# Performance work log

Hardware: AMD Instinct MI355X
Metric: run time of the kernel (lower is better)

## Reference

```python
import jax, jax.numpy as jnp
import numpy as np

BSZ, SEQ, DK = 16, 2048, 64


def setup_inputs() -> dict:
    key = jax.random.key(0)
    kq, kk, kv, kp = jax.random.split(key, 4)
    Q = jax.random.normal(kq, (BSZ, SEQ, DK), dtype=jnp.float32)
    K = jax.random.normal(kk, (BSZ, SEQ, DK), dtype=jnp.float32)
    V = jax.random.normal(kv, (BSZ, SEQ, DK), dtype=jnp.float32)
    # learned relative-position key projection, Parameter(dk, sizeSeq)
    Krelpos = jax.random.normal(kp, (DK, SEQ), dtype=jnp.float32) * (1.0 / np.sqrt(DK))
    return {"Q": Q, "K": K, "V": V, "Krelpos": Krelpos}


def reference(Q, K, V, Krelpos):
    b, S, dk = Q.shape
    # content scores: [b, S, S]
    QK = jnp.einsum('bsd,btd->bst', Q, K)
    # relative-position bias via skew trick
    QP = jnp.einsum('bsd,dt->bst', Q, Krelpos)                     # [b, S, S]
    QP = jnp.concatenate([jnp.zeros((b, S, 1), QP.dtype), QP], axis=2)  # [b, S, S+1]
    QK = QK + QP.reshape(b, S + 1, S)[:, 1:, :]                    # skewed -> [b, S, S]
    # causal mask: -inf strictly above diagonal
    causal = jnp.tril(jnp.ones((S, S), dtype=bool))
    mask = jnp.where(causal, jnp.zeros((), QK.dtype), -jnp.inf)
    A = jax.nn.softmax(QK / jnp.sqrt(jnp.asarray(dk, QK.dtype)) + mask, axis=2)
    # dropout p=0.0 -> identity
    return jnp.einsum('bst,btd->bsd', A, V)
```

## Files before the change

### kernel.cpp

```cpp
#include <hip/hip_runtime.h>
#include <math.h>

#define BSZ 16
#define SEQ 2048
#define DKD 64
#define NTH 256

typedef __attribute__((ext_vector_type(8))) short bf16x8;
typedef __attribute__((ext_vector_type(8))) short short8;
typedef __attribute__((ext_vector_type(4))) float f32x4;

__device__ __forceinline__ short f2bf(float x) {
  union { float f; unsigned u; } c; c.f = x;
  unsigned r = c.u + 0x7fffu + ((c.u >> 16) & 1u);
  return (short)(r >> 16);
}

__device__ __forceinline__ int pkbf(float hi, float lo) {
  return (int)__builtin_amdgcn_perm(__float_as_uint(hi), __float_as_uint(lo), 0x07060302u);
}

#define GLD16(gsrc, ldst)                                                                  \
  __builtin_amdgcn_global_load_lds((const __attribute__((address_space(1))) void*)(gsrc), \
                                   (__attribute__((address_space(3))) void*)(ldst), 16, 0, 0)

#define CH(row, c8) (((row) << 3) + ((c8) ^ ((row) & 7)))


__launch_bounds__(NTH)
__global__ void pre_convert(const float* __restrict__ K, const float* __restrict__ V,
                            const float* __restrict__ P, short* __restrict__ Kbf,
                            short* __restrict__ VTbf, short* __restrict__ PTbf,
                            float* __restrict__ Ozero, float* __restrict__ Lzero) {
  __shared__ short T[64 * 65];
  const int blk = blockIdx.x;
  const int tid = threadIdx.x;
  if (blk < 1024) {
    const int b = blk >> 6, ch = blk & 63;
    const float* Kb = K + ((size_t)(b * SEQ + ch * 32)) * DKD;
    const float* Vb = V + ((size_t)(b * SEQ + ch * 32)) * DKD;
    const int r = tid >> 3, c8 = (tid & 7) << 3;
    float4 a0 = *(const float4*)(Kb + r * DKD + c8);
    float4 a1 = *(const float4*)(Kb + r * DKD + c8 + 4);
    short8 ko;
    ko[0] = f2bf(a0.x); ko[1] = f2bf(a0.y); ko[2] = f2bf(a0.z); ko[3] = f2bf(a0.w);
    ko[4] = f2bf(a1.x); ko[5] = f2bf(a1.y); ko[6] = f2bf(a1.z); ko[7] = f2bf(a1.w);
    *(short8*)(Kbf + ((size_t)(b * SEQ + ch * 32 + r)) * DKD + c8) = ko;
    float4 v0 = *(const float4*)(Vb + r * DKD + c8);
    float4 v1 = *(const float4*)(Vb + r * DKD + c8 + 4);
    T[(c8 + 0) * 33 + r] = f2bf(v0.x); T[(c8 + 1) * 33 + r] = f2bf(v0.y);
    T[(c8 + 2) * 33 + r] = f2bf(v0.z); T[(c8 + 3) * 33 + r] = f2bf(v0.w);
    T[(c8 + 4) * 33 + r] = f2bf(v1.x); T[(c8 + 5) * 33 + r] = f2bf(v1.y);
    T[(c8 + 6) * 33 + r] = f2bf(v1.z); T[(c8 + 7) * 33 + r] = f2bf(v1.w);
    __syncthreads();
    const int d = tid >> 2, q8 = (tid & 3) << 3;
    short8 w;
    #pragma unroll
    for (int j = 0; j < 8; ++j) w[j] = T[d * 33 + q8 + j];
    *(short8*)(VTbf + ((size_t)(b * DKD + d)) * SEQ + ch * 32 + q8) = w;
  } else if (blk < 1056) {
    const int c0 = (blk - 1024) * 64;
    const int d = tid >> 2, cc4 = (tid & 3) << 4;
    #pragma unroll
    for (int j4 = 0; j4 < 4; ++j4) {
      const int c = cc4 + j4 * 4;
      float4 pv = *(const float4*)(P + (size_t)d * SEQ + c0 + c);
      T[(c + 0) * 65 + d] = f2bf(pv.x);
      T[(c + 1) * 65 + d] = f2bf(pv.y);
      T[(c + 2) * 65 + d] = f2bf(pv.z);
      T[(c + 3) * 65 + d] = f2bf(pv.w);
    }
    __syncthreads();
    const int c = tid >> 2, d4 = (tid & 3) << 4;
    short8 w0, w1;
    #pragma unroll
    for (int j = 0; j < 8; ++j) { w0[j] = T[c * 65 + d4 + j]; w1[j] = T[c * 65 + d4 + 8 + j]; }
    short* Po = PTbf + ((size_t)(c0 + c)) * DKD + d4;
    *(short8*)(Po + 0) = w0;
    *(short8*)(Po + 8) = w1;
  } else if (blk == 1056) {
    short8 z = {0, 0, 0, 0, 0, 0, 0, 0};
    short* Po = PTbf + (size_t)SEQ * DKD + tid * 16;
    *(short8*)(Po + 0) = z;
    *(short8*)(Po + 8) = z;
  } else if (blk < 1569) {
    const int u = blk - 1057;
    float4 z = {0.f, 0.f, 0.f, 0.f};
    float4* p = (float4*)(Ozero + (size_t)u * 4096 + tid * 16);
    p[0] = z; p[1] = z; p[2] = z; p[3] = z;
  } else {
    const int u = blk - 1569;
    float4 z = {0.f, 0.f, 0.f, 0.f};
    float4* p = (float4*)(Lzero + (size_t)u * 4096 + tid * 16);
    p[0] = z; p[1] = z; p[2] = z; p[3] = z;
  }
}

__launch_bounds__(NTH, 4)
__global__ void attn_split(const float* __restrict__ Q,
                           const short* __restrict__ Kbf,
                           const short* __restrict__ VTbf,
                           const short* __restrict__ PTbf,
                           float* __restrict__ Oacc,
                           float* __restrict__ Lacc) {
  __shared__ __align__(16) short smem[16384];
  short* Ks  = smem;
  short* VsT = smem + 4096;
  short* PsT = smem + 8192;

  const int tid = threadIdx.x;
  const int lane = tid & 63;
  const int wave = tid >> 6;
  const int l16 = lane & 15;
  const int quad = lane >> 4;

  const int i = blockIdx.x;
  const int qidx = i >> 5;
  const int s = i & 31;
  const int b = s & 15;
  const int h = s >> 4;
  const int qt = (qidx < 16) ? (31 - qidx) : (qidx - 16);
  const int r0 = qt * 64;
  const int m = (qt + 2) >> 1;
  const int kt0 = h ? m : 0;
  const int kt1 = h ? (qt + 1) : m;
  const float SC = 0.125f * 1.4426950408889634f;

  bf16x8 aq[2];
  {
    const float* Qr = Q + ((size_t)(b * SEQ + r0 + wave * 16 + l16)) * DKD + quad * 8;
    #pragma unroll
    for (int ks = 0; ks < 2; ++ks) {
      float4 x = *(const float4*)(Qr + ks * 32);
      float4 y = *(const float4*)(Qr + ks * 32 + 4);
      bf16x8 t;
      t[0] = f2bf(x.x * SC); t[1] = f2bf(x.y * SC); t[2] = f2bf(x.z * SC); t[3] = f2bf(x.w * SC);
      t[4] = f2bf(y.x * SC); t[5] = f2bf(y.y * SC); t[6] = f2bf(y.z * SC); t[7] = f2bf(y.w * SC);
      aq[ks] = t;
    }
  }

  int gsrc[4];
  bool gcar[4];
  #pragma unroll
  for (int r = 0; r < 4; ++r) {
    int o = 15 - (quad * 4 + r);
    int ss = l16 + o;
    gsrc[r] = (quad << 4) | (ss & 15);
    gcar[r] = (ss >= 16);
  }

  union i4v { int4 i; bf16x8 v; };
  i4v ONESu; ONESu.i = make_int4(0x3F803F80, 0x3F803F80, 0x3F803F80, 0x3F803F80);
  i4v S0u, S1u;
  S0u.i = make_int4(0, 0, 0, 0);
  S1u.i = make_int4(0, 0, 0, 0);
  if (quad == (l16 >> 2)) {
    const int j = l16 & 3;
    const int val = 0x3F80 << ((j & 1) * 16);
    if (j < 2) { S0u.i.x = val; S1u.i.z = val; }
    else       { S0u.i.y = val; S1u.i.w = val; }
  }

  f32x4 oacc[4];
  #pragma unroll
  for (int t = 0; t < 4; ++t)
    #pragma unroll
    for (int j = 0; j < 4; ++j) oacc[t][j] = 0.f;
  f32x4 bl;
  #pragma unroll
  for (int j = 0; j < 4; ++j) bl[j] = 0.f;

  const int Blo0 = 31 - qt;

  for (int kt = kt0; kt < kt1; ++kt) {
    const int j0 = kt * 64;
    __syncthreads();

    #pragma unroll
    for (int half = 0; half < 2; ++half) {
      const int ii = wave * 2 + half;
      const int j = ii * 64 + lane;
      {
        const int k = j >> 3, c8 = (j & 7) ^ (k & 7);
        GLD16(Kbf + ((size_t)(b * SEQ + j0 + k)) * DKD + c8 * 8, Ks + ii * 512);
      }
      {
        const int d = j >> 3, c8 = (j & 7) ^ (d & 7);
        GLD16(VTbf + ((size_t)(b * DKD + d)) * SEQ + j0 + c8 * 8, VsT + ii * 512);
      }
    }
    {
      const int Bg = Blo0 + kt + 1;
      #pragma unroll
      for (int half = 0; half < 2; ++half) {
        const int ii = wave * 2 + half;
        const int j = ii * 64 + lane;
        const int c = j >> 3, c8 = (j & 7) ^ (c & 7);
        GLD16(PTbf + ((size_t)(Bg * 64 + c)) * DKD + c8 * 8,
              PsT + ((Bg & 1) << 12) + ii * 512);
      }
      if (kt == kt0) {
        const int Bl = Blo0 + kt0;
        #pragma unroll
        for (int half = 0; half < 2; ++half) {
          const int ii = wave * 2 + half;
          const int j = ii * 64 + lane;
          const int c = j >> 3, c8 = (j & 7) ^ (c & 7);
          GLD16(PTbf + ((size_t)(Bl * 64 + c)) * DKD + c8 * 8,
                PsT + ((Bl & 1) << 12) + ii * 512);
        }
      }
    }
    __syncthreads();

    f32x4 sacc[4];
    #pragma unroll
    for (int t = 0; t < 4; ++t)
      #pragma unroll
      for (int j = 0; j < 4; ++j) sacc[t][j] = 0.f;
    #pragma unroll
    for (int ks = 0; ks < 2; ++ks)
      #pragma unroll
      for (int t = 0; t < 4; ++t) {
        bf16x8 bk = *(const bf16x8*)&Ks[CH(t * 16 + l16, ks * 4 + quad) << 3];
        sacc[t] = __builtin_amdgcn_mfma_f32_16x16x32_bf16(aq[ks], bk, sacc[t], 0, 0, 0);
      }

    float g[5][4];
    #pragma unroll
    for (int tt = 0; tt < 5; ++tt) {
      f32x4 bacc;
      #pragma unroll
      for (int j = 0; j < 4; ++j) bacc[j] = 0.f;
      const int c = (tt + 3 - wave) * 16 + l16;
      const int pan = (Blo0 + kt + (c >> 6)) & 1;
      const int pr = c & 63;
      #pragma unroll
      for (int ks = 0; ks < 2; ++ks) {
        bf16x8 bp = *(const bf16x8*)&PsT[(pan << 12) + (CH(pr, ks * 4 + quad) << 3)];
        bacc = __builtin_amdgcn_mfma_f32_16x16x32_bf16(aq[ks], bp, bacc, 0, 0, 0);
      }
      #pragma unroll
      for (int r = 0; r < 4; ++r) g[tt][r] = __shfl(bacc[r], gsrc[r], 64);
    }

    const bool diag = (kt == qt);
    float e[4][4];
    #pragma unroll
    for (int t = 0; t < 4; ++t)
      #pragma unroll
      for (int r = 0; r < 4; ++r) {
        float sc = sacc[t][r] + (gcar[r] ? g[t + 1][r] : g[t][r]);
        if (diag && (t * 16 + l16 > wave * 16 + quad * 4 + r)) sc = -INFINITY;
        e[t][r] = exp2f(sc);
      }

    i4v ap0, ap1;
    ap0.i.x = pkbf(e[0][1], e[0][0]); ap0.i.y = pkbf(e[0][3], e[0][2]);
    ap0.i.z = pkbf(e[1][1], e[1][0]); ap0.i.w = pkbf(e[1][3], e[1][2]);
    ap1.i.x = pkbf(e[2][1], e[2][0]); ap1.i.y = pkbf(e[2][3], e[2][2]);
    ap1.i.z = pkbf(e[3][1], e[3][0]); ap1.i.w = pkbf(e[3][3], e[3][2]);

    f32x4 zero4;
    #pragma unroll
    for (int j = 0; j < 4; ++j) zero4[j] = 0.f;
    f32x4 Dt[4];
    Dt[0] = __builtin_amdgcn_mfma_f32_16x16x32_bf16(ap0.v, S0u.v, zero4, 0, 0, 0);
    Dt[1] = __builtin_amdgcn_mfma_f32_16x16x32_bf16(ap0.v, S1u.v, zero4, 0, 0, 0);
    Dt[2] = __builtin_amdgcn_mfma_f32_16x16x32_bf16(ap1.v, S0u.v, zero4, 0, 0, 0);
    Dt[3] = __builtin_amdgcn_mfma_f32_16x16x32_bf16(ap1.v, S1u.v, zero4, 0, 0, 0);

    i4v bp0, bp1;
    bp0.i.x = pkbf(Dt[0][1], Dt[0][0]); bp0.i.y = pkbf(Dt[0][3], Dt[0][2]);
    bp0.i.z = pkbf(Dt[1][1], Dt[1][0]); bp0.i.w = pkbf(Dt[1][3], Dt[1][2]);
    bp1.i.x = pkbf(Dt[2][1], Dt[2][0]); bp1.i.y = pkbf(Dt[2][3], Dt[2][2]);
    bp1.i.z = pkbf(Dt[3][1], Dt[3][0]); bp1.i.w = pkbf(Dt[3][3], Dt[3][2]);

    #pragma unroll
    for (int tp = 0; tp < 2; ++tp) {
      const bf16x8 bpk = tp ? bp1.v : bp0.v;
      bl = __builtin_amdgcn_mfma_f32_16x16x32_bf16(ONESu.v, bpk, bl, 0, 0, 0);
      #pragma unroll
      for (int dt = 0; dt < 4; ++dt) {
        const int row = dt * 16 + l16;
        ushort4 lo = *(const ushort4*)&VsT[(CH(row, tp * 4 + (quad >> 1)) << 3) + (quad & 1) * 4];
        ushort4 hi = *(const ushort4*)&VsT[(CH(row, tp * 4 + 2 + (quad >> 1)) << 3) + (quad & 1) * 4];
        bf16x8 av;
        av[0] = (short)lo.x; av[1] = (short)lo.y; av[2] = (short)lo.z; av[3] = (short)lo.w;
        av[4] = (short)hi.x; av[5] = (short)hi.y; av[6] = (short)hi.z; av[7] = (short)hi.w;
        oacc[dt] = __builtin_amdgcn_mfma_f32_16x16x32_bf16(av, bpk, oacc[dt], 0, 0, 0);
      }
    }
  }

  __syncthreads();
  float* Te = (float*)smem;
  #pragma unroll
  for (int dt = 0; dt < 4; ++dt)
    #pragma unroll
    for (int r = 0; r < 4; ++r)
      Te[(wave * 16 + l16) * 65 + dt * 16 + quad * 4 + r] = oacc[dt][r];
  __syncthreads();
  {
    float* Ob = Oacc + ((size_t)(b * SEQ + r0)) * DKD;
    #pragma unroll
    for (int j = 0; j < 16; ++j) {
      const int idx = j * NTH + tid;
      const int row = idx >> 6, col = idx & 63;
      unsafeAtomicAdd(&Ob[(size_t)row * DKD + col], Te[row * 65 + col]);
    }
    if (quad == 0)
      unsafeAtomicAdd(&Lacc[b * SEQ + r0 + wave * 16 + l16], bl[0]);
  }
}

__launch_bounds__(NTH)
__global__ void norm_out(float* __restrict__ O, const float* __restrict__ L) {
  const int tid = threadIdx.x;
  const int row = blockIdx.x * 16 + (tid >> 4);
  const int c4 = (tid & 15) << 2;
  const float rl = 1.0f / L[row];
  float4* p = (float4*)(O + (size_t)row * DKD + c4);
  float4 v = *p;
  v.x *= rl; v.y *= rl; v.z *= rl; v.w *= rl;
  *p = v;
}

extern "C" void kernel_launch(void* const* d_in, const int* in_sizes, int n_in,
                              void* d_out, int out_size, void* d_ws, size_t ws_size,
                              hipStream_t stream) {
  const float* Q = (const float*)d_in[0];
  const float* K = (const float*)d_in[1];
  const float* V = (const float*)d_in[2];
  const float* P = (const float*)d_in[3];
  float* O = (float*)d_out;

  short* Kbf = (short*)d_ws;
  short* VTbf = (short*)((char*)d_ws + 4194304);
  short* PTbf = (short*)((char*)d_ws + 8388608);
  float* Lacc = (float*)((char*)d_ws + 8658944);

  hipLaunchKernelGGL(pre_convert, dim3(1577), dim3(NTH), 0, stream,
                     K, V, P, Kbf, VTbf, PTbf, O, Lacc);
  hipLaunchKernelGGL(attn_split, dim3(1024), dim3(NTH), 0, stream,
                     Q, Kbf, VTbf, PTbf, O, Lacc);
  hipLaunchKernelGGL(norm_out, dim3(BSZ * SEQ / 16), dim3(NTH), 0, stream, O, Lacc);
}
```

Baseline: 134.6 us.

## Split KV range four ways and fuse normalization via last-block counter

Each query tile's key range now goes to four blocks instead of two, doubling the grid for better load balance and occupancy. A per-tile atomic counter lets the last finishing block divide the accumulated output by the softmax sum, which removes the separate norm_out launch. The VT layout is permuted so the PV operand loads as a single 16-byte LDS read. In exchange there are more atomic adds to O and L and an extra threadfence plus counter atomic per block.

```diff
diff --git a/kernel.cpp b/kernel.cpp
--- a/kernel.cpp
+++ b/kernel.cpp
@@ -31,7 +31,8 @@
 __global__ void pre_convert(const float* __restrict__ K, const float* __restrict__ V,
                             const float* __restrict__ P, short* __restrict__ Kbf,
                             short* __restrict__ VTbf, short* __restrict__ PTbf,
-                            float* __restrict__ Ozero, float* __restrict__ Lzero) {
+                            float* __restrict__ Ozero, float* __restrict__ Lzero,
+                            int* __restrict__ cnt) {
   __shared__ short T[64 * 65];
   const int blk = blockIdx.x;
   const int tid = threadIdx.x;
@@ -53,11 +54,14 @@
     T[(c8 + 4) * 33 + r] = f2bf(v1.x); T[(c8 + 5) * 33 + r] = f2bf(v1.y);
     T[(c8 + 6) * 33 + r] = f2bf(v1.z); T[(c8 + 7) * 33 + r] = f2bf(v1.w);
     __syncthreads();
-    const int d = tid >> 2, q8 = (tid & 3) << 3;
+    const int d = tid >> 2, qg = tid & 3;
     short8 w;
     #pragma unroll
-    for (int j = 0; j < 8; ++j) w[j] = T[d * 33 + q8 + j];
-    *(short8*)(VTbf + ((size_t)(b * DKD + d)) * SEQ + ch * 32 + q8) = w;
+    for (int j = 0; j < 4; ++j) {
+      w[j]     = T[d * 33 + qg * 4 + j];
+      w[4 + j] = T[d * 33 + 16 + qg * 4 + j];
+    }
+    *(short8*)(VTbf + ((size_t)(b * DKD + d)) * SEQ + ch * 32 + qg * 8) = w;
   } else if (blk < 1056) {
     const int c0 = (blk - 1024) * 64;
     const int d = tid >> 2, cc4 = (tid & 3) << 4;
@@ -88,11 +92,13 @@
     float4 z = {0.f, 0.f, 0.f, 0.f};
     float4* p = (float4*)(Ozero + (size_t)u * 4096 + tid * 16);
     p[0] = z; p[1] = z; p[2] = z; p[3] = z;
-  } else {
+  } else if (blk < 1577) {
     const int u = blk - 1569;
     float4 z = {0.f, 0.f, 0.f, 0.f};
     float4* p = (float4*)(Lzero + (size_t)u * 4096 + tid * 16);
     p[0] = z; p[1] = z; p[2] = z; p[3] = z;
+  } else {
+    if (tid < 128) ((int4*)cnt)[tid] = make_int4(0, 0, 0, 0);
   }
 }
 
@@ -102,7 +108,8 @@
                            const short* __restrict__ VTbf,
                            const short* __restrict__ PTbf,
                            float* __restrict__ Oacc,
-                           float* __restrict__ Lacc) {
+                           float* __restrict__ Lacc,
+                           int* __restrict__ cnt) {
   __shared__ __align__(16) short smem[16384];
   short* Ks  = smem;
   short* VsT = smem + 4096;
@@ -115,15 +122,14 @@
   const int quad = lane >> 4;
 
   const int i = blockIdx.x;
-  const int qidx = i >> 5;
-  const int s = i & 31;
-  const int b = s & 15;
-  const int h = s >> 4;
+  const int qidx = i >> 6;
+  const int s = i & 63;
+  const int b = s >> 2;
+  const int h = s & 3;
   const int qt = (qidx < 16) ? (31 - qidx) : (qidx - 16);
   const int r0 = qt * 64;
-  const int m = (qt + 2) >> 1;
-  const int kt0 = h ? m : 0;
-  const int kt1 = h ? (qt + 1) : m;
+  const int kt0 = ((qt + 1) * h) >> 2;
+  const int kt1 = ((qt + 1) * (h + 1)) >> 2;
   const float SC = 0.125f * 1.4426950408889634f;
 
   bf16x8 aq[2];
@@ -283,12 +289,7 @@
       bl = __builtin_amdgcn_mfma_f32_16x16x32_bf16(ONESu.v, bpk, bl, 0, 0, 0);
       #pragma unroll
       for (int dt = 0; dt < 4; ++dt) {
-        const int row = dt * 16 + l16;
-        ushort4 lo = *(const ushort4*)&VsT[(CH(row, tp * 4 + (quad >> 1)) << 3) + (quad & 1) * 4];
-        ushort4 hi = *(const ushort4*)&VsT[(CH(row, tp * 4 + 2 + (quad >> 1)) << 3) + (quad & 1) * 4];
-        bf16x8 av;
-        av[0] = (short)lo.x; av[1] = (short)lo.y; av[2] = (short)lo.z; av[3] = (short)lo.w;
-        av[4] = (short)hi.x; av[5] = (short)hi.y; av[6] = (short)hi.z; av[7] = (short)hi.w;
+        bf16x8 av = *(const bf16x8*)&VsT[CH(dt * 16 + l16, tp * 4 + quad) << 3];
         oacc[dt] = __builtin_amdgcn_mfma_f32_16x16x32_bf16(av, bpk, oacc[dt], 0, 0, 0);
       }
     }
@@ -302,8 +303,8 @@
     for (int r = 0; r < 4; ++r)
       Te[(wave * 16 + l16) * 65 + dt * 16 + quad * 4 + r] = oacc[dt][r];
   __syncthreads();
-  {
-    float* Ob = Oacc + ((size_t)(b * SEQ + r0)) * DKD;
+  float* Ob = Oacc + ((size_t)(b * SEQ + r0)) * DKD;
+  if (kt1 > kt0) {
     #pragma unroll
     for (int j = 0; j < 16; ++j) {
       const int idx = j * NTH + tid;
@@ -313,18 +314,31 @@
     if (quad == 0)
       unsafeAtomicAdd(&Lacc[b * SEQ + r0 + wave * 16 + l16], bl[0]);
   }
-}
-
-__launch_bounds__(NTH)
-__global__ void norm_out(float* __restrict__ O, const float* __restrict__ L) {
-  const int tid = threadIdx.x;
-  const int row = blockIdx.x * 16 + (tid >> 4);
-  const int c4 = (tid & 15) << 2;
-  const float rl = 1.0f / L[row];
-  float4* p = (float4*)(O + (size_t)row * DKD + c4);
-  float4 v = *p;
-  v.x *= rl; v.y *= rl; v.z *= rl; v.w *= rl;
-  *p = v;
+
+  __threadfence();
+  __syncthreads();
+  int* flagp = (int*)((char*)smem + 32760);
+  if (tid == 0)
+    *flagp = __hip_atomic_fetch_add(&cnt[b * 32 + qt], 1,
+                                    __ATOMIC_ACQ_REL, __HIP_MEMORY_SCOPE_AGENT);
+  __syncthreads();
+  if (*flagp == 3) {
+    float* Lsh = (float*)smem + 4224;
+    if (tid < 64) {
+      float lv = __hip_atomic_load(&Lacc[b * SEQ + r0 + tid],
+                                   __ATOMIC_RELAXED, __HIP_MEMORY_SCOPE_AGENT);
+      Lsh[tid] = 1.0f / lv;
+    }
+    __syncthreads();
+    #pragma unroll
+    for (int j = 0; j < 16; ++j) {
+      const int idx = j * NTH + tid;
+      const int row = idx >> 6, col = idx & 63;
+      float ov = __hip_atomic_load(&Ob[(size_t)row * DKD + col],
+                                   __ATOMIC_RELAXED, __HIP_MEMORY_SCOPE_AGENT);
+      Ob[(size_t)row * DKD + col] = ov * Lsh[row];
+    }
+  }
 }
 
 extern "C" void kernel_launch(void* const* d_in, const int* in_sizes, int n_in,
@@ -340,10 +354,10 @@
   short* VTbf = (short*)((char*)d_ws + 4194304);
   short* PTbf = (short*)((char*)d_ws + 8388608);
   float* Lacc = (float*)((char*)d_ws + 8658944);
-
-  hipLaunchKernelGGL(pre_convert, dim3(1577), dim3(NTH), 0, stream,
-                     K, V, P, Kbf, VTbf, PTbf, O, Lacc);
-  hipLaunchKernelGGL(attn_split, dim3(1024), dim3(NTH), 0, stream,
-                     Q, Kbf, VTbf, PTbf, O, Lacc);
-  hipLaunchKernelGGL(norm_out, dim3(BSZ * SEQ / 16), dim3(NTH), 0, stream, O, Lacc);
-}
+  int* cnt = (int*)((char*)d_ws + 8790016);
+
+  hipLaunchKernelGGL(pre_convert, dim3(1578), dim3(NTH), 0, stream,
+                     K, V, P, Kbf, VTbf, PTbf, O, Lacc, cnt);
+  hipLaunchKernelGGL(attn_split, dim3(2048), dim3(NTH), 0, stream,
+                     Q, Kbf, VTbf, PTbf, O, Lacc, cnt);
+}
```

New measurement: 374.7 us. 178% more time.
